# Kernel tuning notes

Measured on AMD Instinct MI355X. Metric: run time of the kernel, lower is better.

The kernel has to match this reference:

```python
import jax, jax.numpy as jnp
import numpy as np

N_CELL, N_NET, N_GCELL = 50000, 10000, 20000
E = 100000
D = 32   # hidden_node = hidden_net = hidden_hanna = out_node = out_net
DP = 16  # hidden_pin = hidden_edge feats


def setup_inputs() -> dict:
    key = jax.random.key(0)
    ks = jax.random.split(key, 21)
    f = jax.random.normal
    ri = lambda k, n: jax.random.randint(k, (E,), 0, n, dtype=jnp.int32)
    return {
        'node_feat': f(ks[0], (N_CELL, D), jnp.float32),
        'net_feat': f(ks[1], (N_NET, D), jnp.float32),
        'pin_feat': f(ks[2], (E, DP), jnp.float32),
        'hanna_feat': f(ks[3], (N_GCELL, D), jnp.float32),
        'edge_feat': f(ks[4], (E, DP), jnp.float32),
        'pins_src': ri(ks[5], N_CELL), 'pins_dst': ri(ks[6], N_NET),
        'pinned_src': ri(ks[7], N_NET), 'pinned_dst': ri(ks[8], N_CELL),
        'connect_src': ri(ks[9], N_GCELL), 'connect_dst': ri(ks[10], N_GCELL),
        'pt_src': ri(ks[11], N_CELL), 'pt_dst': ri(ks[12], N_GCELL),
        'pf_src': ri(ks[13], N_GCELL), 'pf_dst': ri(ks[14], N_CELL),
        'W_net': f(ks[15], (D, D)) * 0.1, 'b_net': jnp.zeros((D,), jnp.float32),
        'W_topo': f(ks[16], (DP, D * D)) * 0.1, 'b_topo': jnp.zeros((D * D,), jnp.float32),
        'W_pins': f(ks[17], (D, D)) * 0.1, 'b_pins': jnp.zeros((D,), jnp.float32),
        'W_connect': f(ks[18], (D, D)) * 0.1, 'b_connect': jnp.zeros((D,), jnp.float32),
        'W_pt': f(ks[19], (D, D)) * 0.1, 'b_pt': jnp.zeros((D,), jnp.float32),
        'b_pinned': jnp.zeros((D,), jnp.float32), 'b_pf': jnp.zeros((D,), jnp.float32),
    }


def _deg(idx, n):
    # clamped degree, as DGL clamps to min 1
    return jnp.maximum(jax.ops.segment_sum(jnp.ones_like(idx, jnp.float32), idx, n), 1.0)


def graph_conv(h_src, W, b, src, dst, n_src, n_dst):
    # DGL GraphConv with norm='both': D_out^{-1/2} gather -> sum -> D_in^{-1/2}, then W, b
    feat = (h_src * _deg(src, n_src)[:, None] ** -0.5) @ W
    agg = jax.ops.segment_sum(feat[src], dst, n_dst)
    return agg * _deg(dst, n_dst)[:, None] ** -0.5 + b


def nn_conv(h_src, efeat, W_topo, b_topo, bias, src, dst, n_dst):
    # DGL NNConv (aggregator='mean'): per-edge weight from edge_func, mean over in-edges
    d_in = h_src.shape[1]
    w = (efeat @ W_topo + b_topo).reshape(-1, d_in, bias.shape[0])  # (E, d_in, d_out)
    m = jnp.einsum('ei,eio->eo', h_src[src], w)
    return jax.ops.segment_sum(m, dst, n_dst) / _deg(dst, n_dst)[:, None] + bias


def reference(node_feat, net_feat, pin_feat, hanna_feat, edge_feat,
              pins_src, pins_dst, pinned_src, pinned_dst, connect_src, connect_dst,
              pt_src, pt_dst, pf_src, pf_dst,
              W_net, b_net, W_topo, b_topo, W_pins, b_pins,
              W_connect, b_connect, W_pt, b_pt, b_pinned, b_pf):
    # 'pins': cell -> net (GraphConv)
    h_net = graph_conv(node_feat, W_pins, b_pins, pins_src, pins_dst, N_CELL, N_NET)
    # 'pinned': net -> cell (NNConv) + 'point-from': gcell -> cell (NNConv); agg='sum'
    h_cell = (nn_conv(net_feat, pin_feat, W_topo, b_topo, b_pinned, pinned_src, pinned_dst, N_CELL)
              + nn_conv(hanna_feat, edge_feat, W_topo, b_topo, b_pf, pf_src, pf_dst, N_CELL))
    # 'connect': gcell -> gcell + 'point-to': cell -> gcell (GraphConvs); agg='sum'
    h_gcell = (graph_conv(hanna_feat, W_connect, b_connect, connect_src, connect_dst, N_GCELL, N_GCELL)
               + graph_conv(node_feat, W_pt, b_pt, pt_src, pt_dst, N_CELL, N_GCELL))
    return (h_cell, h_net + net_feat @ W_net + b_net, h_gcell)
```

## Files before the change

### kernel.cpp

```cpp
#include <hip/hip_runtime.h>

typedef unsigned short u16;
typedef unsigned int u32;

#define NC 50000
#define NN 10000
#define NG 20000
#define NE 100000
#define NSCAN 150016
#define NBLK 74


__device__ __forceinline__ float bflo(u32 a) { return __uint_as_float(a << 16); }
__device__ __forceinline__ float bfhi(u32 a) { return __uint_as_float(a & 0xFFFF0000u); }
__device__ __forceinline__ u16 fbf(float f) {
  u32 u = __float_as_uint(f);
  return (u16)((u + 0x7FFFu + ((u >> 16) & 1u)) >> 16);
}

__global__ __launch_bounds__(256) void k_hist(
    const int* __restrict__ pins_src, const int* __restrict__ pins_dst,
    const int* __restrict__ pinned_dst, const int* __restrict__ pf_dst,
    const int* __restrict__ connect_src, const int* __restrict__ connect_dst,
    const int* __restrict__ pt_src, const int* __restrict__ pt_dst,
    int* __restrict__ hist, int* __restrict__ srccnt) {
  int e = blockIdx.x * 256 + threadIdx.x;
  if (e >= NE) return;
  atomicAdd(&hist[pins_dst[e]], 1);
  atomicAdd(&hist[10000 + connect_dst[e]], 1);
  atomicAdd(&hist[30000 + pt_dst[e]], 1);
  atomicAdd(&hist[50000 + pinned_dst[e]], 1);
  atomicAdd(&hist[100000 + pf_dst[e]], 1);
  atomicAdd(&srccnt[pins_src[e]], 1);
  atomicAdd(&srccnt[50000 + connect_src[e]], 1);
  atomicAdd(&srccnt[70000 + pt_src[e]], 1);
}

__global__ __launch_bounds__(256) void k_scan1(
    const int* __restrict__ cnt, int* __restrict__ bsum) {
  __shared__ int sm[256];
  int b = blockIdx.x, tid = threadIdx.x;
  int base = b * 2048 + tid * 8;
  int tot = 0;
#pragma unroll
  for (int j = 0; j < 8; j++) {
    int i = base + j;
    tot += (i < NSCAN) ? cnt[i] : 0;
  }
  sm[tid] = tot;
  __syncthreads();
  for (int off = 128; off > 0; off >>= 1) {
    if (tid < off) sm[tid] += sm[tid + off];
    __syncthreads();
  }
  if (tid == 0) bsum[b] = sm[0];
}

__global__ void k_scan2(int* __restrict__ bsum) {
  if (threadIdx.x == 0 && blockIdx.x == 0) {
    int run = 0;
    for (int b = 0; b < NBLK; b++) {
      int v = bsum[b];
      bsum[b] = run;
      run += v;
    }
  }
}

__global__ __launch_bounds__(256) void k_scan3(
    const int* __restrict__ cnt, const int* __restrict__ boff,
    int* __restrict__ bases) {
  __shared__ int sm[256];
  int b = blockIdx.x, tid = threadIdx.x;
  int base = b * 2048 + tid * 8;
  int v[8];
  int tot = 0;
#pragma unroll
  for (int j = 0; j < 8; j++) {
    int i = base + j;
    v[j] = (i < NSCAN) ? cnt[i] : 0;
    tot += v[j];
  }
  sm[tid] = tot;
  __syncthreads();
  for (int off = 1; off < 256; off <<= 1) {
    int add = (tid >= off) ? sm[tid - off] : 0;
    __syncthreads();
    sm[tid] += add;
    __syncthreads();
  }
  int excl = sm[tid] - tot + boff[b];
#pragma unroll
  for (int j = 0; j < 8; j++) {
    int i = base + j;
    if (i < NSCAN) bases[i] = excl;
    excl += v[j];
  }
}

__global__ __launch_bounds__(256) void k_fill(
    const int* __restrict__ pins_dst, const int* __restrict__ connect_dst,
    const int* __restrict__ pt_dst, const int* __restrict__ pinned_dst,
    const int* __restrict__ pf_dst,
    const int* __restrict__ bases, int* __restrict__ cursor,
    int* __restrict__ idx_all) {
  int t = blockIdx.x * 256 + threadIdx.x;
  if (t >= 5 * NE) return;
  int r = t / NE, e = t - r * NE;
  const int* dsts = r == 0 ? pins_dst : r == 1 ? connect_dst
                   : r == 2 ? pt_dst : r == 3 ? pinned_dst : pf_dst;
  int off = r == 0 ? 0 : r == 1 ? 10000 : r == 2 ? 30000 : r == 3 ? 50000 : 100000;
  int g = off + dsts[e];
  int pos = atomicAdd(&cursor[g], 1);
  idx_all[bases[g] + pos] = e;
}

__global__ __launch_bounds__(512) void k_transform(
    const float* __restrict__ feat_net, const float* __restrict__ feat_han,
    const float* __restrict__ W_topo,
    u16* __restrict__ T_net, u16* __restrict__ T_han) {
  bool han = blockIdx.x >= 313;
  const float* feat = han ? feat_han : feat_net;
  u16* T = han ? T_han : T_net;
  int n = han ? NG : NN;
  int blk = han ? (blockIdx.x - 313) : blockIdx.x;
  int j = threadIdx.x;
  int p = j & 15, o = j >> 4;
  float w[32];
#pragma unroll
  for (int i = 0; i < 32; i++) w[i] = W_topo[p * 1024 + i * 32 + o];

  __shared__ float hs[4][32];
  int s0 = blk * 32;
  int s1 = min(s0 + 32, n);
  for (int s = s0; s < s1; s += 4) {
    __syncthreads();
    if (threadIdx.x < 128) {
      int r = threadIdx.x >> 5, i = threadIdx.x & 31;
      int sn = s + r;
      hs[r][i] = (sn < s1) ? feat[(size_t)sn * 32 + i] : 0.f;
    }
    __syncthreads();
#pragma unroll
    for (int r = 0; r < 4; r++) {
      int sn = s + r;
      if (sn >= s1) break;
      float acc = 0.f;
#pragma unroll
      for (int i = 0; i < 32; i++) acc += hs[r][i] * w[i];
      T[(size_t)sn * 512 + j] = fbf(acc);
    }
  }
}

__global__ __launch_bounds__(256) void k_C(
    const float* __restrict__ feat_net, const float* __restrict__ feat_han,
    const float* __restrict__ b_topo,
    float* __restrict__ C_net, float* __restrict__ C_han) {
  int t = blockIdx.x * 256 + threadIdx.x;
  if (t >= (NN + NG) * 32) return;
  int s2 = t >> 5, o = t & 31;
  bool han = s2 >= NN;
  const float* feat = han ? feat_han : feat_net;
  float* C = han ? C_han : C_net;
  int s = han ? s2 - NN : s2;
  float acc = 0.f;
#pragma unroll 8
  for (int i = 0; i < 32; i++)
    acc += feat[(size_t)s * 32 + i] * b_topo[i * 32 + o];
  C[(size_t)s * 32 + o] = acc;
}

__global__ __launch_bounds__(256) void k_gc_gather(
    const int* __restrict__ hist, const int* __restrict__ bases,
    const int* __restrict__ idx_all, const int* __restrict__ srccnt,
    const int* __restrict__ pins_src, const int* __restrict__ connect_src,
    const int* __restrict__ pt_src,
    const float* __restrict__ node_feat, const float* __restrict__ hanna_feat,
    float* __restrict__ S_net, float* __restrict__ S_conn, float* __restrict__ S_pt) {
  int t = blockIdx.x * 256 + threadIdx.x;
  int rr = t >> 5, o = t & 31;
  if (rr >= 50000) return;
  int rel = (rr >= 10000) + (rr >= 30000);
  const int* srcarr = rel == 0 ? pins_src : rel == 1 ? connect_src : pt_src;
  const float* feat = (rel == 1) ? hanna_feat : node_feat;
  const int* scnt = srccnt + (rel == 0 ? 0 : rel == 1 ? 50000 : 70000);
  float* S = rel == 0 ? S_net + (size_t)rr * 32
           : rel == 1 ? S_conn + (size_t)(rr - 10000) * 32
                      : S_pt + (size_t)(rr - 30000) * 32;
  int base = bases[rr], deg = hist[rr];
  float acc = 0.f;
  for (int k = 0; k < deg; k++) {
    int e = idx_all[base + k];
    int s = srcarr[e];
    float w = rsqrtf(fmaxf((float)scnt[s], 1.f));
    acc += feat[(size_t)s * 32 + o] * w;
  }
  S[o] = acc;
}

__global__ __launch_bounds__(256) void k_nn_gather(
    const int* __restrict__ hist, const int* __restrict__ bases,
    const int* __restrict__ idx_all,
    const int* __restrict__ pinned_src, const int* __restrict__ pf_src,
    const float* __restrict__ pin_feat, const float* __restrict__ edge_feat,
    const u16* __restrict__ T_net, const u16* __restrict__ T_han,
    const float* __restrict__ C_net, const float* __restrict__ C_han,
    const float* __restrict__ b_pinned, const float* __restrict__ b_pf,
    float* __restrict__ out) {
  int t = blockIdx.x * 256 + threadIdx.x;
  int d = t >> 5, o = t & 31;
  if (d >= NC) return;
  float a0 = 0.f, a1 = 0.f;
  {
    int g = 50000 + d;
    int base = bases[g], deg = hist[g];
    for (int k = 0; k < deg; k++) {
      int e = idx_all[base + k];
      int s = pinned_src[e];
      const float4* efp = reinterpret_cast<const float4*>(pin_feat + (size_t)e * 16);
      float4 ea = efp[0], eb = efp[1], ec = efp[2], ed = efp[3];
      const uint4* tp = reinterpret_cast<const uint4*>(T_net + (size_t)s * 512 + o * 16);
      uint4 ta = tp[0], tb = tp[1];
      float m = C_net[(size_t)s * 32 + o];
      m += ea.x * bflo(ta.x) + ea.y * bfhi(ta.x) + ea.z * bflo(ta.y) + ea.w * bfhi(ta.y);
      m += eb.x * bflo(ta.z) + eb.y * bfhi(ta.z) + eb.z * bflo(ta.w) + eb.w * bfhi(ta.w);
      m += ec.x * bflo(tb.x) + ec.y * bfhi(tb.x) + ec.z * bflo(tb.y) + ec.w * bfhi(tb.y);
      m += ed.x * bflo(tb.z) + ed.y * bfhi(tb.z) + ed.z * bflo(tb.w) + ed.w * bfhi(tb.w);
      a0 += m;
    }
    a0 /= fmaxf((float)deg, 1.f);
  }
  {
    int g = 100000 + d;
    int base = bases[g], deg = hist[g];
    for (int k = 0; k < deg; k++) {
      int e = idx_all[base + k];
      int s = pf_src[e];
      const float4* efp = reinterpret_cast<const float4*>(edge_feat + (size_t)e * 16);
      float4 ea = efp[0], eb = efp[1], ec = efp[2], ed = efp[3];
      const uint4* tp = reinterpret_cast<const uint4*>(T_han + (size_t)s * 512 + o * 16);
      uint4 ta = tp[0], tb = tp[1];
      float m = C_han[(size_t)s * 32 + o];
      m += ea.x * bflo(ta.x) + ea.y * bfhi(ta.x) + ea.z * bflo(ta.y) + ea.w * bfhi(ta.y);
      m += eb.x * bflo(ta.z) + eb.y * bfhi(ta.z) + eb.z * bflo(ta.w) + eb.w * bfhi(ta.w);
      m += ec.x * bflo(tb.x) + ec.y * bfhi(tb.x) + ec.z * bflo(tb.y) + ec.w * bfhi(tb.y);
      m += ed.x * bflo(tb.z) + ed.y * bfhi(tb.z) + ed.z * bflo(tb.w) + ed.w * bfhi(tb.w);
      a1 += m;
    }
    a1 /= fmaxf((float)deg, 1.f);
  }
  out[(size_t)d * 32 + o] = a0 + a1 + b_pinned[o] + b_pf[o];
}

__global__ __launch_bounds__(256) void k_fin(
    const int* __restrict__ hist,
    const float* __restrict__ S_net, const float* __restrict__ net_feat,
    const float* __restrict__ W_pins, const float* __restrict__ b_pins,
    const float* __restrict__ W_net, const float* __restrict__ b_net,
    const float* __restrict__ S_conn, const float* __restrict__ S_pt,
    const float* __restrict__ W_connect, const float* __restrict__ b_connect,
    const float* __restrict__ W_pt, const float* __restrict__ b_pt,
    float* __restrict__ out) {
  __shared__ float Wa[1024], Wb[1024];
  int b = blockIdx.x;
  if (b < 1250) {
    for (int k = threadIdx.x; k < 1024; k += 256) {
      Wa[k] = W_pins[k];
      Wb[k] = W_net[k];
    }
    __syncthreads();
    int t = b * 256 + threadIdx.x;
    int r = t >> 5, o = t & 31;
    float a1 = 0.f, a2 = 0.f;
#pragma unroll 8
    for (int i = 0; i < 32; i++) {
      a1 += S_net[(size_t)r * 32 + i] * Wa[i * 32 + o];
      a2 += net_feat[(size_t)r * 32 + i] * Wb[i * 32 + o];
    }
    out[1600000 + t] = a1 * rsqrtf(fmaxf((float)hist[r], 1.f)) + b_pins[o] +
                       a2 + b_net[o];
    return;
  }
  for (int k = threadIdx.x; k < 1024; k += 256) {
    Wa[k] = W_connect[k];
    Wb[k] = W_pt[k];
  }
  __syncthreads();
  int t = (b - 1250) * 256 + threadIdx.x;
  int r = t >> 5, o = t & 31;
  float a1 = 0.f, a2 = 0.f;
#pragma unroll 8
  for (int i = 0; i < 32; i++) {
    a1 += S_conn[(size_t)r * 32 + i] * Wa[i * 32 + o];
    a2 += S_pt[(size_t)r * 32 + i] * Wb[i * 32 + o];
  }
  out[1920000 + t] = a1 * rsqrtf(fmaxf((float)hist[10000 + r], 1.f)) + b_connect[o] +
                     a2 * rsqrtf(fmaxf((float)hist[30000 + r], 1.f)) + b_pt[o];
}

extern "C" void kernel_launch(void* const* d_in, const int* in_sizes, int n_in,
                              void* d_out, int out_size, void* d_ws, size_t ws_size,
                              hipStream_t stream) {
  const float* node_feat  = (const float*)d_in[0];
  const float* net_feat   = (const float*)d_in[1];
  const float* pin_feat   = (const float*)d_in[2];
  const float* hanna_feat = (const float*)d_in[3];
  const float* edge_feat  = (const float*)d_in[4];
  const int* pins_src    = (const int*)d_in[5];
  const int* pins_dst    = (const int*)d_in[6];
  const int* pinned_src  = (const int*)d_in[7];
  const int* pinned_dst  = (const int*)d_in[8];
  const int* connect_src = (const int*)d_in[9];
  const int* connect_dst = (const int*)d_in[10];
  const int* pt_src      = (const int*)d_in[11];
  const int* pt_dst      = (const int*)d_in[12];
  const int* pf_src      = (const int*)d_in[13];
  const int* pf_dst      = (const int*)d_in[14];
  const float* W_net     = (const float*)d_in[15];
  const float* b_net     = (const float*)d_in[16];
  const float* W_topo    = (const float*)d_in[17];
  const float* b_topo    = (const float*)d_in[18];
  const float* W_pins    = (const float*)d_in[19];
  const float* b_pins    = (const float*)d_in[20];
  const float* W_connect = (const float*)d_in[21];
  const float* b_connect = (const float*)d_in[22];
  const float* W_pt      = (const float*)d_in[23];
  const float* b_pt      = (const float*)d_in[24];
  const float* b_pinned  = (const float*)d_in[25];
  const float* b_pf      = (const float*)d_in[26];
  float* out = (float*)d_out;

  int* wi = (int*)d_ws;
  int* hist    = wi + 0;
  int* cursor  = wi + 150016;
  int* srccnt  = wi + 300032;
  int* bases   = wi + 420032;
  int* bsum    = wi + 570064;
  int* idx_all = wi + 570192;
  float* wf = (float*)d_ws;
  float* S_net  = wf + 1070192;
  float* S_conn = wf + 1390192;
  float* S_pt   = wf + 2030192;
  float* C_net  = wf + 2670192;
  float* C_han  = wf + 2990192;
  u16* T_net = (u16*)((char*)d_ws + 14520832);
  u16* T_han = (u16*)((char*)d_ws + 14520832 + 10240000);

  hipMemsetAsync(d_ws, 0, 420032 * sizeof(int), stream);

  k_hist<<<(NE + 255) / 256, 256, 0, stream>>>(
      pins_src, pins_dst, pinned_dst, pf_dst, connect_src, connect_dst,
      pt_src, pt_dst, hist, srccnt);

  k_scan1<<<NBLK, 256, 0, stream>>>(hist, bsum);
  k_scan2<<<1, 64, 0, stream>>>(bsum);
  k_scan3<<<NBLK, 256, 0, stream>>>(hist, bsum, bases);

  k_fill<<<(5 * NE + 255) / 256, 256, 0, stream>>>(
      pins_dst, connect_dst, pt_dst, pinned_dst, pf_dst, bases, cursor, idx_all);

  k_transform<<<938, 512, 0, stream>>>(net_feat, hanna_feat, W_topo, T_net, T_han);

  k_C<<<((NN + NG) * 32 + 255) / 256, 256, 0, stream>>>(
      net_feat, hanna_feat, b_topo, C_net, C_han);

  k_gc_gather<<<(50000 * 32) / 256, 256, 0, stream>>>(
      hist, bases, idx_all, srccnt, pins_src, connect_src, pt_src,
      node_feat, hanna_feat, S_net, S_conn, S_pt);

  k_nn_gather<<<(NC * 32) / 256, 256, 0, stream>>>(
      hist, bases, idx_all, pinned_src, pf_src, pin_feat, edge_feat,
      T_net, T_han, C_net, C_han, b_pinned, b_pf, out);

  k_fin<<<3750, 256, 0, stream>>>(
      hist, S_net, net_feat, W_pins, b_pins, W_net, b_net,
      S_conn, S_pt, W_connect, b_connect, W_pt, b_pt, out);
}
```

Baseline: 332.7 us.

## Fuse transform, bias and histogram into one front kernel; merge NN gather with finalize

```diff
diff --git a/kernel.cpp b/kernel.cpp
--- a/kernel.cpp
+++ b/kernel.cpp
@@ -18,13 +18,82 @@
   return (u16)((u + 0x7FFFu + ((u >> 16) & 1u)) >> 16);
 }
 
-__global__ __launch_bounds__(256) void k_hist(
+__device__ __forceinline__ float nn_msg(int e, int s, const float* __restrict__ ef,
+                                        const u16* __restrict__ T,
+                                        const float* __restrict__ C, int o) {
+  const float4* efp = reinterpret_cast<const float4*>(ef + (size_t)e * 16);
+  float4 ea = efp[0], eb = efp[1], ec = efp[2], ed = efp[3];
+  const uint4* tp = reinterpret_cast<const uint4*>(T + (size_t)s * 512 + o * 16);
+  uint4 ta = tp[0], tb = tp[1];
+  float m = C[(size_t)s * 32 + o];
+  m += ea.x * bflo(ta.x) + ea.y * bfhi(ta.x) + ea.z * bflo(ta.y) + ea.w * bfhi(ta.y);
+  m += eb.x * bflo(ta.z) + eb.y * bfhi(ta.z) + eb.z * bflo(ta.w) + eb.w * bfhi(ta.w);
+  m += ec.x * bflo(tb.x) + ec.y * bfhi(tb.x) + ec.z * bflo(tb.y) + ec.w * bfhi(tb.y);
+  m += ed.x * bflo(tb.z) + ed.y * bfhi(tb.z) + ed.z * bflo(tb.w) + ed.w * bfhi(tb.w);
+  return m;
+}
+
+__global__ __launch_bounds__(512) void k_front(
+    const float* __restrict__ feat_net, const float* __restrict__ feat_han,
+    const float* __restrict__ W_topo, const float* __restrict__ b_topo,
+    u16* __restrict__ T_net, u16* __restrict__ T_han,
+    float* __restrict__ C_net, float* __restrict__ C_han,
     const int* __restrict__ pins_src, const int* __restrict__ pins_dst,
     const int* __restrict__ pinned_dst, const int* __restrict__ pf_dst,
     const int* __restrict__ connect_src, const int* __restrict__ connect_dst,
     const int* __restrict__ pt_src, const int* __restrict__ pt_dst,
     int* __restrict__ hist, int* __restrict__ srccnt) {
-  int e = blockIdx.x * 256 + threadIdx.x;
+  int b = blockIdx.x;
+  if (b < 938) {
+    bool han = b >= 313;
+    const float* feat = han ? feat_han : feat_net;
+    u16* T = han ? T_han : T_net;
+    int n = han ? NG : NN;
+    int blk = han ? b - 313 : b;
+    int j = threadIdx.x;
+    int p = j & 15, o = j >> 4;
+    float w[32];
+#pragma unroll
+    for (int i = 0; i < 32; i++) w[i] = W_topo[p * 1024 + i * 32 + o];
+    int s0 = blk * 32;
+    int s1 = min(s0 + 32, n);
+    int sn = s0;
+    for (; sn + 1 < s1; sn += 2) {
+      const float* h0 = feat + (size_t)sn * 32;
+      const float* h1 = h0 + 32;
+      float a0 = 0.f, a1 = 0.f;
+#pragma unroll
+      for (int i = 0; i < 32; i++) {
+        a0 += h0[i] * w[i];
+        a1 += h1[i] * w[i];
+      }
+      T[(size_t)sn * 512 + j] = fbf(a0);
+      T[(size_t)(sn + 1) * 512 + j] = fbf(a1);
+    }
+    if (sn < s1) {
+      const float* h0 = feat + (size_t)sn * 32;
+      float a0 = 0.f;
+#pragma unroll
+      for (int i = 0; i < 32; i++) a0 += h0[i] * w[i];
+      T[(size_t)sn * 512 + j] = fbf(a0);
+    }
+    return;
+  }
+  if (b < 2813) {
+    int t = (b - 938) * 512 + threadIdx.x;
+    int s2 = t >> 5, o = t & 31;
+    bool han = s2 >= NN;
+    const float* feat = han ? feat_han : feat_net;
+    float* C = han ? C_han : C_net;
+    int s = han ? s2 - NN : s2;
+    float acc = 0.f;
+#pragma unroll 8
+    for (int i = 0; i < 32; i++)
+      acc += feat[(size_t)s * 32 + i] * b_topo[i * 32 + o];
+    C[(size_t)s * 32 + o] = acc;
+    return;
+  }
+  int e = (b - 2813) * 512 + threadIdx.x;
   if (e >= NE) return;
   atomicAdd(&hist[pins_dst[e]], 1);
   atomicAdd(&hist[10000 + connect_dst[e]], 1);
@@ -56,22 +125,20 @@
   if (tid == 0) bsum[b] = sm[0];
 }
 
-__global__ void k_scan2(int* __restrict__ bsum) {
-  if (threadIdx.x == 0 && blockIdx.x == 0) {
-    int run = 0;
-    for (int b = 0; b < NBLK; b++) {
-      int v = bsum[b];
-      bsum[b] = run;
-      run += v;
-    }
-  }
-}
-
 __global__ __launch_bounds__(256) void k_scan3(
-    const int* __restrict__ cnt, const int* __restrict__ boff,
+    const int* __restrict__ cnt, const int* __restrict__ bsum,
     int* __restrict__ bases) {
   __shared__ int sm[256];
+  __shared__ int carry;
   int b = blockIdx.x, tid = threadIdx.x;
+  if (tid == 0) {
+    int run = 0;
+    for (int i = 0; i < NBLK; i++) {
+      if (i == b) break;
+      run += bsum[i];
+    }
+    carry = run;
+  }
   int base = b * 2048 + tid * 8;
   int v[8];
   int tot = 0;
@@ -89,7 +156,7 @@
     sm[tid] += add;
     __syncthreads();
   }
-  int excl = sm[tid] - tot + boff[b];
+  int excl = sm[tid] - tot + carry;
 #pragma unroll
   for (int j = 0; j < 8; j++) {
     int i = base + j;
@@ -98,13 +165,13 @@
   }
 }
 
-__global__ __launch_bounds__(256) void k_fill(
+__global__ __launch_bounds__(512) void k_fill(
     const int* __restrict__ pins_dst, const int* __restrict__ connect_dst,
     const int* __restrict__ pt_dst, const int* __restrict__ pinned_dst,
     const int* __restrict__ pf_dst,
     const int* __restrict__ bases, int* __restrict__ cursor,
     int* __restrict__ idx_all) {
-  int t = blockIdx.x * 256 + threadIdx.x;
+  int t = blockIdx.x * 512 + threadIdx.x;
   if (t >= 5 * NE) return;
   int r = t / NE, e = t - r * NE;
   const int* dsts = r == 0 ? pins_dst : r == 1 ? connect_dst
@@ -115,72 +182,15 @@
   idx_all[bases[g] + pos] = e;
 }
 
-__global__ __launch_bounds__(512) void k_transform(
-    const float* __restrict__ feat_net, const float* __restrict__ feat_han,
-    const float* __restrict__ W_topo,
-    u16* __restrict__ T_net, u16* __restrict__ T_han) {
-  bool han = blockIdx.x >= 313;
-  const float* feat = han ? feat_han : feat_net;
-  u16* T = han ? T_han : T_net;
-  int n = han ? NG : NN;
-  int blk = han ? (blockIdx.x - 313) : blockIdx.x;
-  int j = threadIdx.x;
-  int p = j & 15, o = j >> 4;
-  float w[32];
-#pragma unroll
-  for (int i = 0; i < 32; i++) w[i] = W_topo[p * 1024 + i * 32 + o];
-
-  __shared__ float hs[4][32];
-  int s0 = blk * 32;
-  int s1 = min(s0 + 32, n);
-  for (int s = s0; s < s1; s += 4) {
-    __syncthreads();
-    if (threadIdx.x < 128) {
-      int r = threadIdx.x >> 5, i = threadIdx.x & 31;
-      int sn = s + r;
-      hs[r][i] = (sn < s1) ? feat[(size_t)sn * 32 + i] : 0.f;
-    }
-    __syncthreads();
-#pragma unroll
-    for (int r = 0; r < 4; r++) {
-      int sn = s + r;
-      if (sn >= s1) break;
-      float acc = 0.f;
-#pragma unroll
-      for (int i = 0; i < 32; i++) acc += hs[r][i] * w[i];
-      T[(size_t)sn * 512 + j] = fbf(acc);
-    }
-  }
-}
-
-__global__ __launch_bounds__(256) void k_C(
-    const float* __restrict__ feat_net, const float* __restrict__ feat_han,
-    const float* __restrict__ b_topo,
-    float* __restrict__ C_net, float* __restrict__ C_han) {
-  int t = blockIdx.x * 256 + threadIdx.x;
-  if (t >= (NN + NG) * 32) return;
-  int s2 = t >> 5, o = t & 31;
-  bool han = s2 >= NN;
-  const float* feat = han ? feat_han : feat_net;
-  float* C = han ? C_han : C_net;
-  int s = han ? s2 - NN : s2;
-  float acc = 0.f;
-#pragma unroll 8
-  for (int i = 0; i < 32; i++)
-    acc += feat[(size_t)s * 32 + i] * b_topo[i * 32 + o];
-  C[(size_t)s * 32 + o] = acc;
-}
-
-__global__ __launch_bounds__(256) void k_gc_gather(
+__global__ __launch_bounds__(512) void k_gc_gather(
     const int* __restrict__ hist, const int* __restrict__ bases,
     const int* __restrict__ idx_all, const int* __restrict__ srccnt,
     const int* __restrict__ pins_src, const int* __restrict__ connect_src,
     const int* __restrict__ pt_src,
     const float* __restrict__ node_feat, const float* __restrict__ hanna_feat,
     float* __restrict__ S_net, float* __restrict__ S_conn, float* __restrict__ S_pt) {
-  int t = blockIdx.x * 256 + threadIdx.x;
+  int t = blockIdx.x * 512 + threadIdx.x;
   int rr = t >> 5, o = t & 31;
-  if (rr >= 50000) return;
   int rel = (rr >= 10000) + (rr >= 30000);
   const int* srcarr = rel == 0 ? pins_src : rel == 1 ? connect_src : pt_src;
   const float* feat = (rel == 1) ? hanna_feat : node_feat;
@@ -190,16 +200,23 @@
                       : S_pt + (size_t)(rr - 30000) * 32;
   int base = bases[rr], deg = hist[rr];
   float acc = 0.f;
-  for (int k = 0; k < deg; k++) {
+  int k = 0;
+  for (; k + 1 < deg; k += 2) {
+    int ea = idx_all[base + k], eb = idx_all[base + k + 1];
+    int sa = srcarr[ea], sb = srcarr[eb];
+    float wa = rsqrtf(fmaxf((float)scnt[sa], 1.f));
+    float wb = rsqrtf(fmaxf((float)scnt[sb], 1.f));
+    acc += feat[(size_t)sa * 32 + o] * wa + feat[(size_t)sb * 32 + o] * wb;
+  }
+  if (k < deg) {
     int e = idx_all[base + k];
     int s = srcarr[e];
-    float w = rsqrtf(fmaxf((float)scnt[s], 1.f));
-    acc += feat[(size_t)s * 32 + o] * w;
+    acc += feat[(size_t)s * 32 + o] * rsqrtf(fmaxf((float)scnt[s], 1.f));
   }
   S[o] = acc;
 }
 
-__global__ __launch_bounds__(256) void k_nn_gather(
+__global__ __launch_bounds__(512) void k_tail(
     const int* __restrict__ hist, const int* __restrict__ bases,
     const int* __restrict__ idx_all,
     const int* __restrict__ pinned_src, const int* __restrict__ pf_src,
@@ -207,54 +224,6 @@
     const u16* __restrict__ T_net, const u16* __restrict__ T_han,
     const float* __restrict__ C_net, const float* __restrict__ C_han,
     const float* __restrict__ b_pinned, const float* __restrict__ b_pf,
-    float* __restrict__ out) {
-  int t = blockIdx.x * 256 + threadIdx.x;
-  int d = t >> 5, o = t & 31;
-  if (d >= NC) return;
-  float a0 = 0.f, a1 = 0.f;
-  {
-    int g = 50000 + d;
-    int base = bases[g], deg = hist[g];
-    for (int k = 0; k < deg; k++) {
-      int e = idx_all[base + k];
-      int s = pinned_src[e];
-      const float4* efp = reinterpret_cast<const float4*>(pin_feat + (size_t)e * 16);
-      float4 ea = efp[0], eb = efp[1], ec = efp[2], ed = efp[3];
-      const uint4* tp = reinterpret_cast<const uint4*>(T_net + (size_t)s * 512 + o * 16);
-      uint4 ta = tp[0], tb = tp[1];
-      float m = C_net[(size_t)s * 32 + o];
-      m += ea.x * bflo(ta.x) + ea.y * bfhi(ta.x) + ea.z * bflo(ta.y) + ea.w * bfhi(ta.y);
-      m += eb.x * bflo(ta.z) + eb.y * bfhi(ta.z) + eb.z * bflo(ta.w) + eb.w * bfhi(ta.w);
-      m += ec.x * bflo(tb.x) + ec.y * bfhi(tb.x) + ec.z * bflo(tb.y) + ec.w * bfhi(tb.y);
-      m += ed.x * bflo(tb.z) + ed.y * bfhi(tb.z) + ed.z * bflo(tb.w) + ed.w * bfhi(tb.w);
-      a0 += m;
-    }
-    a0 /= fmaxf((float)deg, 1.f);
-  }
-  {
-    int g = 100000 + d;
-    int base = bases[g], deg = hist[g];
-    for (int k = 0; k < deg; k++) {
-      int e = idx_all[base + k];
-      int s = pf_src[e];
-      const float4* efp = reinterpret_cast<const float4*>(edge_feat + (size_t)e * 16);
-      float4 ea = efp[0], eb = efp[1], ec = efp[2], ed = efp[3];
-      const uint4* tp = reinterpret_cast<const uint4*>(T_han + (size_t)s * 512 + o * 16);
-      uint4 ta = tp[0], tb = tp[1];
-      float m = C_han[(size_t)s * 32 + o];
-      m += ea.x * bflo(ta.x) + ea.y * bfhi(ta.x) + ea.z * bflo(ta.y) + ea.w * bfhi(ta.y);
-      m += eb.x * bflo(ta.z) + eb.y * bfhi(ta.z) + eb.z * bflo(ta.w) + eb.w * bfhi(ta.w);
-      m += ec.x * bflo(tb.x) + ec.y * bfhi(tb.x) + ec.z * bflo(tb.y) + ec.w * bfhi(tb.y);
-      m += ed.x * bflo(tb.z) + ed.y * bfhi(tb.z) + ed.z * bflo(tb.w) + ed.w * bfhi(tb.w);
-      a1 += m;
-    }
-    a1 /= fmaxf((float)deg, 1.f);
-  }
-  out[(size_t)d * 32 + o] = a0 + a1 + b_pinned[o] + b_pf[o];
-}
-
-__global__ __launch_bounds__(256) void k_fin(
-    const int* __restrict__ hist,
     const float* __restrict__ S_net, const float* __restrict__ net_feat,
     const float* __restrict__ W_pins, const float* __restrict__ b_pins,
     const float* __restrict__ W_net, const float* __restrict__ b_net,
@@ -264,13 +233,52 @@
     float* __restrict__ out) {
   __shared__ float Wa[1024], Wb[1024];
   int b = blockIdx.x;
-  if (b < 1250) {
-    for (int k = threadIdx.x; k < 1024; k += 256) {
+  if (b < 3125) {
+    int t = b * 512 + threadIdx.x;
+    int d = t >> 5, o = t & 31;
+    float a0 = 0.f, a1 = 0.f;
+    {
+      int g = 50000 + d;
+      int base = bases[g], deg = hist[g];
+      int k = 0;
+      for (; k + 1 < deg; k += 2) {
+        int ea = idx_all[base + k], eb = idx_all[base + k + 1];
+        int sa = pinned_src[ea], sb = pinned_src[eb];
+        a0 += nn_msg(ea, sa, pin_feat, T_net, C_net, o) +
+              nn_msg(eb, sb, pin_feat, T_net, C_net, o);
+      }
+      if (k < deg) {
+        int e = idx_all[base + k];
+        a0 += nn_msg(e, pinned_src[e], pin_feat, T_net, C_net, o);
+      }
+      a0 /= fmaxf((float)deg, 1.f);
+    }
+    {
+      int g = 100000 + d;
+      int base = bases[g], deg = hist[g];
+      int k = 0;
+      for (; k + 1 < deg; k += 2) {
+        int ea = idx_all[base + k], eb = idx_all[base + k + 1];
+        int sa = pf_src[ea], sb = pf_src[eb];
+        a1 += nn_msg(ea, sa, edge_feat, T_han, C_han, o) +
+              nn_msg(eb, sb, edge_feat, T_han, C_han, o);
+      }
+      if (k < deg) {
+        int e = idx_all[base + k];
+        a1 += nn_msg(e, pf_src[e], edge_feat, T_han, C_han, o);
+      }
+      a1 /= fmaxf((float)deg, 1.f);
+    }
+    out[(size_t)d * 32 + o] = a0 + a1 + b_pinned[o] + b_pf[o];
+    return;
+  }
+  if (b < 3750) {
+    for (int k = threadIdx.x; k < 1024; k += 512) {
       Wa[k] = W_pins[k];
       Wb[k] = W_net[k];
     }
     __syncthreads();
-    int t = b * 256 + threadIdx.x;
+    int t = (b - 3125) * 512 + threadIdx.x;
     int r = t >> 5, o = t & 31;
     float a1 = 0.f, a2 = 0.f;
 #pragma unroll 8
@@ -282,12 +290,12 @@
                        a2 + b_net[o];
     return;
   }
-  for (int k = threadIdx.x; k < 1024; k += 256) {
+  for (int k = threadIdx.x; k < 1024; k += 512) {
     Wa[k] = W_connect[k];
     Wb[k] = W_pt[k];
   }
   __syncthreads();
-  int t = (b - 1250) * 256 + threadIdx.x;
+  int t = (b - 3750) * 512 + threadIdx.x;
   int r = t >> 5, o = t & 31;
   float a1 = 0.f, a2 = 0.f;
 #pragma unroll 8
@@ -349,31 +357,24 @@
 
   hipMemsetAsync(d_ws, 0, 420032 * sizeof(int), stream);
 
-  k_hist<<<(NE + 255) / 256, 256, 0, stream>>>(
+  k_front<<<3009, 512, 0, stream>>>(
+      net_feat, hanna_feat, W_topo, b_topo, T_net, T_han, C_net, C_han,
       pins_src, pins_dst, pinned_dst, pf_dst, connect_src, connect_dst,
       pt_src, pt_dst, hist, srccnt);
 
   k_scan1<<<NBLK, 256, 0, stream>>>(hist, bsum);
-  k_scan2<<<1, 64, 0, stream>>>(bsum);
   k_scan3<<<NBLK, 256, 0, stream>>>(hist, bsum, bases);
 
-  k_fill<<<(5 * NE + 255) / 256, 256, 0, stream>>>(
+  k_fill<<<(5 * NE + 511) / 512, 512, 0, stream>>>(
       pins_dst, connect_dst, pt_dst, pinned_dst, pf_dst, bases, cursor, idx_all);
 
-  k_transform<<<938, 512, 0, stream>>>(net_feat, hanna_feat, W_topo, T_net, T_han);
-
-  k_C<<<((NN + NG) * 32 + 255) / 256, 256, 0, stream>>>(
-      net_feat, hanna_feat, b_topo, C_net, C_han);
-
-  k_gc_gather<<<(50000 * 32) / 256, 256, 0, stream>>>(
+  k_gc_gather<<<3125, 512, 0, stream>>>(
       hist, bases, idx_all, srccnt, pins_src, connect_src, pt_src,
       node_feat, hanna_feat, S_net, S_conn, S_pt);
 
-  k_nn_gather<<<(NC * 32) / 256, 256, 0, stream>>>(
+  k_tail<<<5000, 512, 0, stream>>>(
       hist, bases, idx_all, pinned_src, pf_src, pin_feat, edge_feat,
-      T_net, T_han, C_net, C_han, b_pinned, b_pf, out);
-
-  k_fin<<<3750, 256, 0, stream>>>(
-      hist, S_net, net_feat, W_pins, b_pins, W_net, b_net,
+      T_net, T_han, C_net, C_han, b_pinned, b_pf,
+      S_net, net_feat, W_pins, b_pins, W_net, b_net,
       S_conn, S_pt, W_connect, b_connect, W_pt, b_pt, out);
 }
```

Result: faster. 303.9 us (-8.6%).
